# Performance work log

Hardware: AMD Instinct MI355X
Metric: run time of the kernel (lower is better)

## Reference

```python
import jax, jax.numpy as jnp
import numpy as np

B, T, E, H, O = 32, 512, 768, 3132, 19


def _ln(x, g, b, eps=1e-5):
    m = x.mean(-1, keepdims=True)
    v = x.var(-1, keepdims=True)
    return (x - m) / jnp.sqrt(v + eps) * g + b


def _cell(x, h, wih, bih, whh, bhh):
    # torch.nn.RNNCell with tanh nonlinearity
    return jnp.tanh(x @ wih.T + bih + h @ whh.T + bhh)


def _mha(seq, wqkv, bqkv, wo, bo):
    # seq: [T,B,D]; single-head torch MultiheadAttention (eval mode, no dropout)
    D = seq.shape[-1]
    qkv = seq @ wqkv.T + bqkv
    q, k, v = jnp.split(qkv, 3, axis=-1)
    scores = jnp.einsum('tbd,sbd->bts', q, k) / jnp.sqrt(jnp.asarray(D, seq.dtype))
    a = jax.nn.softmax(scores, axis=-1)
    ctx = jnp.einsum('bts,sbd->tbd', a, v)
    return ctx @ wo.T + bo


def setup_inputs() -> dict:
    key = jax.random.key(0)
    ks = jax.random.split(key, 12)
    s = lambda k, shape: jax.random.normal(k, shape, jnp.float32) * 0.02
    return {
        'x': jax.random.normal(ks[0], (B, T, E), jnp.float32),
        'in_g': jnp.ones((E,), jnp.float32), 'in_b': jnp.zeros((E,), jnp.float32),
        'w_ih1': s(ks[1], (H, E)), 'w_hh1': s(ks[2], (H, H)),
        'b_ih1': jnp.zeros((H,), jnp.float32), 'b_hh1': jnp.zeros((H,), jnp.float32),
        'ln1_g': jnp.ones((H,), jnp.float32), 'ln1_b': jnp.zeros((H,), jnp.float32),
        'w_ih2': s(ks[3], (E, H)), 'w_hh2': s(ks[4], (E, E)),
        'b_ih2': jnp.zeros((E,), jnp.float32), 'b_hh2': jnp.zeros((E,), jnp.float32),
        'mha1_wqkv': s(ks[5], (3 * H, H)), 'mha1_bqkv': jnp.zeros((3 * H,), jnp.float32),
        'mha1_wo': s(ks[6], (H, H)), 'mha1_bo': jnp.zeros((H,), jnp.float32),
        'mha2_wqkv': s(ks[7], (3 * E, E)), 'mha2_bqkv': jnp.zeros((3 * E,), jnp.float32),
        'mha2_wo': s(ks[8], (E, E)), 'mha2_bo': jnp.zeros((E,), jnp.float32),
        'w_cls': s(ks[9], (O, E)), 'b_cls': jnp.zeros((O,), jnp.float32),
    }


def reference(x, in_g, in_b, w_ih1, w_hh1, b_ih1, b_hh1, ln1_g, ln1_b,
              w_ih2, w_hh2, b_ih2, b_hh2,
              mha1_wqkv, mha1_bqkv, mha1_wo, mha1_bo,
              mha2_wqkv, mha2_bqkv, mha2_wo, mha2_bo, w_cls, b_cls):
    b = x.shape[0]
    xn = _ln(x, in_g, in_b)            # input_norm
    xs = jnp.swapaxes(xn, 0, 1)        # [T,B,E]
    h1_0 = jnp.zeros((b, w_ih1.shape[0]), x.dtype)
    h2_0 = jnp.zeros((b, w_ih2.shape[0]), x.dtype)

    def step(carry, xt):
        h1, h2 = carry
        h1 = _ln(_cell(xt, h1, w_ih1, b_ih1, w_hh1, b_hh1), ln1_g, ln1_b)
        h2 = _cell(h1, h2, w_ih2, b_ih2, w_hh2, b_hh2)
        return (h1, h2), (h1, h2)

    _, (h1s, h2s) = jax.lax.scan(step, (h1_0, h2_0), xs)  # [T,B,H], [T,B,E]
    ctx1 = _mha(h1s, mha1_wqkv, mha1_bqkv, mha1_wo, mha1_bo)  # dropout is identity in eval
    ctx2 = _mha(h2s, mha2_wqkv, mha2_bqkv, mha2_wo, mha2_bo)
    # the original second loop overwrites h1/h2 each t; only t = T-1 survives
    h1 = _cell(xs[-1], ctx1[-1], w_ih1, b_ih1, w_hh1, b_hh1)
    h2 = _cell(h1, ctx2[-1], w_ih2, b_ih2, w_hh2, b_hh2)
    return h2 @ w_cls.T + b_cls
```

## Files before the change

kernel.cpp:

```cpp
#include <hip/hip_runtime.h>
#include <cstdint>
#include <cmath>

#define BB 32
#define TT 512
#define EE 768
#define HH 3132
#define HP 3136
#define OO 19

#define NBLK 451
#define NTHR 256
#define WP 456
#define AP 232


#define PT(t) (((t) * 331) & 511)

typedef __attribute__((ext_vector_type(8))) short s8v;
typedef __attribute__((ext_vector_type(4))) float f4v;
typedef __attribute__((ext_vector_type(8))) unsigned short u16x8;

__device__ __forceinline__ unsigned short f2bf(float f) {
    uint32_t u = __float_as_uint(f);
    uint32_t r = u + 0x7FFFu + ((u >> 16) & 1u);
    return (unsigned short)(r >> 16);
}
__device__ __forceinline__ float bf2f(unsigned short h) {
    return __uint_as_float(((uint32_t)h) << 16);
}

#define MFMA(a, b, c) __builtin_amdgcn_mfma_f32_16x16x32_bf16((a), (b), (c), 0, 0, 0)

__device__ __forceinline__ f4v ld4_sc(const void* p) {
    f4v v;
    asm volatile("global_load_dwordx4 %0, %1, off sc0 sc1" : "=v"(v) : "v"(p) : "memory");
    return v;
}
#define WAITV() do { asm volatile("s_waitcnt vmcnt(0)" ::: "memory"); \
                     __builtin_amdgcn_sched_barrier(0); } while (0)
__device__ __forceinline__ void st_sc(float* p, float v) {
    __hip_atomic_store(p, v, __ATOMIC_RELAXED, __HIP_MEMORY_SCOPE_AGENT);
}
__device__ __forceinline__ void st16_sc(void* p, u16x8 v) {
    asm volatile("global_store_dwordx4 %0, %1, off sc0 sc1" :: "v"(p), "v"(v) : "memory");
}
__device__ __forceinline__ void st8_sc(void* p, uint2 v) {
    asm volatile("global_store_dwordx2 %0, %1, off sc0 sc1" :: "v"(p), "v"(v) : "memory");
}

struct PP {
    const unsigned short *xw1hi, *xw1lo;
    const unsigned short *whh1hi, *whh1lo, *wih2, *whh2;
    const float *b1c, *b2c, *gpad, *bepad;
    unsigned short *h1hist, *h2hist;
    unsigned short *h1nlo, *h2lo;
    float *part1, *part2;
    unsigned int *grp;
    unsigned int *epoch;
};

__device__ __forceinline__ void gbar(const PP& p, unsigned int k) {
    __syncthreads();
    asm volatile("s_waitcnt vmcnt(0)" ::: "memory");
    if (threadIdx.x == 0)
        __hip_atomic_fetch_add(&p.grp[(blockIdx.x & 63) * 32], 1u,
                               __ATOMIC_RELAXED, __HIP_MEMORY_SCOPE_AGENT);
    if (blockIdx.x == 0) {
        if (threadIdx.x < 64) {
            unsigned int mem = 7u + (threadIdx.x < (NBLK & 63) ? 1u : 0u);
            unsigned int tgt = mem * k;
            long g = 0;
            while (__hip_atomic_load(&p.grp[threadIdx.x * 32], __ATOMIC_RELAXED,
                                     __HIP_MEMORY_SCOPE_AGENT) < tgt) {
                __builtin_amdgcn_s_sleep(2);
                if (++g > (1L << 16)) break;
            }
        }
        __syncthreads();
        if (threadIdx.x == 0)
            __hip_atomic_store(p.epoch, k, __ATOMIC_RELAXED, __HIP_MEMORY_SCOPE_AGENT);
    } else {
        if (threadIdx.x == 0) {
            long g = 0;
            while (__hip_atomic_load(p.epoch, __ATOMIC_RELAXED,
                                     __HIP_MEMORY_SCOPE_AGENT) < k) {
                __builtin_amdgcn_s_sleep(2);
                if (++g > (1L << 16)) break;
            }
        }
    }
    __syncthreads();
    asm volatile("" ::: "memory");
}

__global__ __launch_bounds__(NTHR, 2) void persist_k(PP p) {
    __shared__ unsigned short Wlds[64][WP];
    __shared__ unsigned short Alds[32][AP];
    __shared__ float redS[4], redQ[4];
    const int blk = blockIdx.x, tid = threadIdx.x;
    const int wid = tid >> 6, lane = tid & 63;
    const int r = lane & 15, kg = lane >> 4;
    unsigned int bar = 0;

    const int t1nt = blk / 7,          t1ks = blk % 7;
    const int t2i  = blk - 343,        t2nt = t2i / 7, t2ks = t2i % 7;
    const int t3i  = blk - 427,        t3nt = t3i / 2, t3kh = t3i % 2;

    if (blk < 343) {
        const unsigned short* src = p.whh1hi + (size_t)(t1nt * 64) * HP + t1ks * 448;
        #pragma unroll
        for (int i = 0; i < 14; ++i) {
            int idx = tid + i * 256;
            int row = idx / 56, c8 = idx % 56;
            *(uint4*)&Wlds[row][c8 * 8] = *(const uint4*)(src + (size_t)row * HP + c8 * 8);
        }
    } else if (blk < 427) {
        const unsigned short* src = p.wih2 + (size_t)(t2nt * 64) * HP + t2ks * 448;
        #pragma unroll
        for (int i = 0; i < 14; ++i) {
            int idx = tid + i * 256;
            int row = idx / 56, c8 = idx % 56;
            *(uint4*)&Wlds[row][c8 * 8] = *(const uint4*)(src + (size_t)row * HP + c8 * 8);
        }
    } else {
        const unsigned short* src = p.whh2 + (size_t)(t3nt * 64) * EE + t3kh * 384;
        #pragma unroll
        for (int i = 0; i < 12; ++i) {
            int idx = tid + i * 256;
            int row = idx / 48, c8 = idx % 48;
            *(uint4*)&Wlds[row][c8 * 8] = *(const uint4*)(src + (size_t)row * EE + c8 * 8);
        }
    }
    __syncthreads();

    for (int t = 0; t <= TT; ++t) {
        if (blk < 343) {
            if (t >= 1 && t <= TT - 1) {
                f4v a0 = {0.f,0.f,0.f,0.f}, a1 = {0.f,0.f,0.f,0.f};
                const unsigned short* Wl = p.whh1lo + (size_t)(t1nt * 64 + wid * 16 + r) * HP + t1ks * 448 + kg * 8;
                const unsigned short* ringb = p.h1hist + (size_t)PT(t - 1) * BB * HP + t1ks * 448 + kg * 8;
                for (int hx = 0; hx < 2; ++hx) {
                    __syncthreads();
                    {
                        f4v lv[4];
                        #pragma unroll
                        for (int i = 0; i < 4; ++i) {
                            int idx = tid + i * 256;
                            int row = (idx < 896) ? idx / 28 : 0;
                            int c8  = (idx < 896) ? idx % 28 : 0;
                            lv[i] = ld4_sc(p.h1nlo + (size_t)row * HP + t1ks * 448 + hx * 224 + c8 * 8);
                        }
                        WAITV();
                        #pragma unroll
                        for (int i = 0; i < 4; ++i) {
                            int idx = tid + i * 256;
                            if (idx < 896) {
                                int row = idx / 28, c8 = idx % 28;
                                *(f4v*)&Alds[row][c8 * 8] = lv[i];
                            }
                        }
                    }
                    __syncthreads();
                    const unsigned short* Ah0 = ringb + (size_t)r * HP + hx * 224;
                    const unsigned short* Ah1 = ringb + (size_t)(r + 16) * HP + hx * 224;
                    const unsigned short* Wlh = Wl + hx * 224;
                    #pragma unroll
                    for (int kb = 0; kb < 7; ++kb) {
                        s8v bh  = *(const s8v*)&Wlds[wid * 16 + r][hx * 224 + kb * 32 + kg * 8];
                        s8v bl  = *(const s8v*)(Wlh + kb * 32);
                        s8v ah0 = *(const s8v*)(Ah0 + kb * 32);
                        s8v ah1 = *(const s8v*)(Ah1 + kb * 32);
                        s8v al0 = *(const s8v*)&Alds[r][kb * 32 + kg * 8];
                        s8v al1 = *(const s8v*)&Alds[r + 16][kb * 32 + kg * 8];
                        a0 = MFMA(ah0, bh, a0); a1 = MFMA(ah1, bh, a1);
                        a0 = MFMA(al0, bh, a0); a1 = MFMA(al1, bh, a1);
                        a0 = MFMA(ah0, bl, a0); a1 = MFMA(ah1, bl, a1);
                    }
                }
                int ncol = t1nt * 64 + wid * 16 + r;
                float* pp1 = p.part1 + (size_t)t1ks * BB * HP + ncol;
                #pragma unroll
                for (int q = 0; q < 4; ++q) {
                    st_sc(pp1 + (size_t)(kg * 4 + q) * HP,      a0[q]);
                    st_sc(pp1 + (size_t)(kg * 4 + q + 16) * HP, a1[q]);
                }
            }
        } else if (blk < 427) {
            if (t >= 1) {
                const unsigned short* ringb = p.h1hist + (size_t)PT(t - 1) * BB * HP + t2ks * 448 + kg * 8;
                const unsigned short* Ah0 = ringb + (size_t)r * HP;
                const unsigned short* Ah1 = ringb + (size_t)(r + 16) * HP;
                f4v a0 = {0.f,0.f,0.f,0.f}, a1 = {0.f,0.f,0.f,0.f};
                #pragma unroll
                for (int kb = 0; kb < 14; ++kb) {
                    s8v bh  = *(const s8v*)&Wlds[wid * 16 + r][kb * 32 + kg * 8];
                    s8v ah0 = *(const s8v*)(Ah0 + kb * 32);
                    s8v ah1 = *(const s8v*)(Ah1 + kb * 32);
                    a0 = MFMA(ah0, bh, a0); a1 = MFMA(ah1, bh, a1);
                }
                int ncol = t2nt * 64 + wid * 16 + r;
                float* pp2 = p.part2 + (size_t)t2ks * BB * EE + ncol;
                #pragma unroll
                for (int q = 0; q < 4; ++q) {
                    st_sc(pp2 + (size_t)(kg * 4 + q) * EE,      a0[q]);
                    st_sc(pp2 + (size_t)(kg * 4 + q + 16) * EE, a1[q]);
                }
            }
        } else {
            if (t >= 2) {
                const unsigned short* Hh = p.h2hist + (size_t)PT(t - 2) * BB * EE + t3kh * 384 + kg * 8;
                const unsigned short* Hl = p.h2lo + t3kh * 384 + kg * 8;
                f4v a0 = {0.f,0.f,0.f,0.f}, a1 = {0.f,0.f,0.f,0.f};
                #pragma unroll
                for (int c = 0; c < 2; ++c) {
                    f4v v0l[6], v1l[6];
                    #pragma unroll
                    for (int u = 0; u < 6; ++u) {
                        int kb = c * 6 + u;
                        v0l[u] = ld4_sc(Hl + (size_t)r * EE + kb * 32);
                        v1l[u] = ld4_sc(Hl + (size_t)(r + 16) * EE + kb * 32);
                    }
                    WAITV();
                    #pragma unroll
                    for (int u = 0; u < 6; ++u) {
                        int kb = c * 6 + u;
                        s8v bh  = *(const s8v*)&Wlds[wid * 16 + r][kb * 32 + kg * 8];
                        s8v ah0 = *(const s8v*)(Hh + (size_t)r * EE + kb * 32);
                        s8v ah1 = *(const s8v*)(Hh + (size_t)(r + 16) * EE + kb * 32);
                        a0 = MFMA(ah0, bh, a0);
                        a0 = MFMA(__builtin_bit_cast(s8v, v0l[u]), bh, a0);
                        a1 = MFMA(ah1, bh, a1);
                        a1 = MFMA(__builtin_bit_cast(s8v, v1l[u]), bh, a1);
                    }
                }
                int ncol = t3nt * 64 + wid * 16 + r;
                float* pp2 = p.part2 + (size_t)(7 + t3kh) * BB * EE + ncol;
                #pragma unroll
                for (int q = 0; q < 4; ++q) {
                    st_sc(pp2 + (size_t)(kg * 4 + q) * EE,      a0[q]);
                    st_sc(pp2 + (size_t)(kg * 4 + q + 16) * EE, a1[q]);
                }
            }
        }
        gbar(p, ++bar);

        if (blk < 32) {
            if (t <= TT - 1) {
                const int b = blk;
                const int nb = tid * 16;
                const bool act = (tid < 196);
                float acc[16];
                float s = 0.f, s2 = 0.f;
                if (act) {
                    #pragma unroll
                    for (int k4 = 0; k4 < 4; ++k4) {
                        f4v bb = *(const f4v*)(p.b1c + nb + k4 * 4);
                        #pragma unroll
                        for (int e = 0; e < 4; ++e) acc[k4 * 4 + e] = bb[e];
                    }
                    const u16x8* xh = (const u16x8*)(p.xw1hi + ((size_t)t * BB + b) * HP + nb);
                    const u16x8* xl = (const u16x8*)(p.xw1lo + ((size_t)t * BB + b) * HP + nb);
                    u16x8 h0v = xh[0], h1v = xh[1], l0v = xl[0], l1v = xl[1];
                    #pragma unroll
                    for (int j = 0; j < 8; ++j) acc[j]     += bf2f(h0v[j]) + bf2f(l0v[j]);
                    #pragma unroll
                    for (int j = 0; j < 8; ++j) acc[8 + j] += bf2f(h1v[j]) + bf2f(l1v[j]);
                    if (t > 0) {
                        {
                            f4v tmp[16];
                            #pragma unroll
                            for (int sl = 0; sl < 4; ++sl) {
                                const float* base = p.part1 + ((size_t)sl * BB + b) * HP + nb;
                                #pragma unroll
                                for (int k4 = 0; k4 < 4; ++k4) tmp[sl * 4 + k4] = ld4_sc(base + k4 * 4);
                            }
                            WAITV();
                            #pragma unroll
                            for (int sl = 0; sl < 4; ++sl)
                                #pragma unroll
                                for (int k4 = 0; k4 < 4; ++k4)
                                    #pragma unroll
                                    for (int e = 0; e < 4; ++e) acc[k4 * 4 + e] += tmp[sl * 4 + k4][e];
                        }
                        {
                            f4v tmp[12];
                            #pragma unroll
                            for (int sl = 0; sl < 3; ++sl) {
                                const float* base = p.part1 + ((size_t)(sl + 4) * BB + b) * HP + nb;
                                #pragma unroll
                                for (int k4 = 0; k4 < 4; ++k4) tmp[sl * 4 + k4] = ld4_sc(base + k4 * 4);
                            }
                            WAITV();
                            #pragma unroll
                            for (int sl = 0; sl < 3; ++sl)
                                #pragma unroll
                                for (int k4 = 0; k4 < 4; ++k4)
                                    #pragma unroll
                                    for (int e = 0; e < 4; ++e) acc[k4 * 4 + e] += tmp[sl * 4 + k4][e];
                        }
                    }
                    #pragma unroll
                    for (int j = 0; j < 16; ++j) {
                        if (nb + j < HH) {
                            float v = tanhf(acc[j]);
                            acc[j] = v; s += v; s2 += v * v;
                        } else acc[j] = 0.f;
                    }
                }
                for (int o = 32; o; o >>= 1) { s += __shfl_xor(s, o); s2 += __shfl_xor(s2, o); }
                if (lane == 0) { redS[wid] = s; redQ[wid] = s2; }
                __syncthreads();
                float S  = redS[0] + redS[1] + redS[2] + redS[3];
                float S2 = redQ[0] + redQ[1] + redQ[2] + redQ[3];
                float mm = S / (float)HH;
                float inv = rsqrtf(S2 / (float)HH - mm * mm + 1e-5f);
                __syncthreads();
                if (act) {
                    u16x8 ho0, ho1, lo0, lo1;
                    #pragma unroll
                    for (int k4 = 0; k4 < 4; ++k4) {
                        f4v gv = *(const f4v*)(p.gpad + nb + k4 * 4);
                        f4v bv = *(const f4v*)(p.bepad + nb + k4 * 4);
                        #pragma unroll
                        for (int e = 0; e < 4; ++e) {
                            int j = k4 * 4 + e, n = nb + j;
                            float o = (n < HH) ? (acc[j] - mm) * inv * gv[e] + bv[e] : 0.f;
                            unsigned short hb = f2bf(o);
                            unsigned short lb = f2bf(o - bf2f(hb));
                            if (j < 8) { ho0[j] = hb; lo0[j] = lb; }
                            else       { ho1[j - 8] = hb; lo1[j - 8] = lb; }
                        }
                    }
                    unsigned short* dh = p.h1hist + ((size_t)PT(t) * BB + b) * HP + nb;
                    unsigned short* dl = p.h1nlo + (size_t)b * HP + nb;
                    st16_sc(dh, ho0); st16_sc(dh + 8, ho1);
                    st16_sc(dl, lo0); st16_sc(dl + 8, lo1);
                }
            }
        } else if (blk < 64) {
            if (t >= 1) {
                const int b = blk - 32;
                if (tid < 192) {
                    const int nb = tid * 4;
                    f4v a4 = *(const f4v*)(p.b2c + nb);
                    f4v tp[9];
                    #pragma unroll
                    for (int sl = 0; sl < 9; ++sl)
                        tp[sl] = ld4_sc(p.part2 + ((size_t)sl * BB + b) * EE + nb);
                    WAITV();
                    #pragma unroll
                    for (int sl = 0; sl < 9; ++sl) {
                        float w = (t == 1 && sl >= 7) ? 0.f : 1.f;
                        #pragma unroll
                        for (int e = 0; e < 4; ++e) a4[e] += w * tp[sl][e];
                    }
                    unsigned short hb4[4], lb4[4];
                    #pragma unroll
                    for (int e = 0; e < 4; ++e) {
                        float v = tanhf(a4[e]);
                        hb4[e] = f2bf(v); lb4[e] = f2bf(v - bf2f(hb4[e]));
                    }
                    uint2 hp_, lp_;
                    hp_.x = (unsigned)hb4[0] | ((unsigned)hb4[1] << 16);
                    hp_.y = (unsigned)hb4[2] | ((unsigned)hb4[3] << 16);
                    lp_.x = (unsigned)lb4[0] | ((unsigned)lb4[1] << 16);
                    lp_.y = (unsigned)lb4[2] | ((unsigned)lb4[3] << 16);
                    st8_sc(p.h2hist + ((size_t)PT(t - 1) * BB + b) * EE + nb, hp_);
                    st8_sc(p.h2lo + (size_t)b * EE + nb, lp_);
                }
            }
        }
        gbar(p, ++bar);
    }
}

__global__ void ln_x_k(const float* __restrict__ x, const float* __restrict__ g,
                       const float* __restrict__ be, unsigned short* __restrict__ xnhi,
                       unsigned short* __restrict__ xnlo) {
    int bt = blockIdx.x;
    int b = bt >> 9, t = bt & 511;
    const float* row = x + ((size_t)b * TT + t) * EE;
    int tid = threadIdx.x;
    float v0 = row[tid], v1 = row[tid + 256], v2 = row[tid + 512];
    float s = v0 + v1 + v2, s2 = v0 * v0 + v1 * v1 + v2 * v2;
    for (int o = 32; o; o >>= 1) { s += __shfl_xor(s, o); s2 += __shfl_xor(s2, o); }
    __shared__ float r1[4], r2[4];
    int wid = tid >> 6, lane = tid & 63;
    if (lane == 0) { r1[wid] = s; r2[wid] = s2; }
    __syncthreads();
    s = r1[0] + r1[1] + r1[2] + r1[3];
    s2 = r2[0] + r2[1] + r2[2] + r2[3];
    float m = s / (float)EE, var = s2 / (float)EE - m * m;
    float inv = rsqrtf(var + 1e-5f);
    size_t ro = ((size_t)t * BB + b) * EE;
    float vals[3] = {v0, v1, v2};
#pragma unroll
    for (int i = 0; i < 3; i++) {
        int e = tid + i * 256;
        float o = (vals[i] - m) * inv * g[e] + be[e];
        unsigned short hb = f2bf(o);
        xnhi[ro + e] = hb;
        xnlo[ro + e] = f2bf(o - bf2f(hb));
    }
}

__global__ void castpad_k(const float* __restrict__ in, int N, int K,
                          unsigned short* __restrict__ out, int Np, int Kp) {
    size_t gid = (size_t)blockIdx.x * 256 + threadIdx.x;
    if (gid >= (size_t)Np * Kp) return;
    int n = (int)(gid / Kp), k = (int)(gid % Kp);
    out[gid] = (n < N && k < K) ? f2bf(in[(size_t)n * K + k]) : (unsigned short)0;
}

__global__ void castsplit_k(const float* __restrict__ in, int N, int K,
                            unsigned short* __restrict__ hi, unsigned short* __restrict__ lo,
                            int Np, int Kp) {
    size_t gid = (size_t)blockIdx.x * 256 + threadIdx.x;
    if (gid >= (size_t)Np * Kp) return;
    int n = (int)(gid / Kp), k = (int)(gid % Kp);
    float v = (n < N && k < K) ? in[(size_t)n * K + k] : 0.0f;
    unsigned short hb = f2bf(v);
    hi[gid] = hb;
    lo[gid] = f2bf(v - bf2f(hb));
}

__global__ void transcast_k(const float* __restrict__ in, int R, int C,
                            unsigned short* __restrict__ out, int Rp, int Cp) {
    __shared__ float tile[32][33];
    int c0 = blockIdx.x * 32, r0 = blockIdx.y * 32;
    int tx = threadIdx.x & 31, ty = threadIdx.x >> 5;
    for (int i = 0; i < 4; i++) {
        int r = r0 + ty + i * 8, c = c0 + tx;
        tile[ty + i * 8][tx] = (r < R && c < C) ? in[(size_t)r * C + c] : 0.0f;
    }
    __syncthreads();
    for (int i = 0; i < 4; i++) {
        int c = c0 + ty + i * 8, r = r0 + tx;
        if (c < Cp && r < Rp) out[(size_t)c * Rp + r] = f2bf(tile[tx][ty + i * 8]);
    }
}

__global__ void biascomb_k(const float* a, const float* b, float* o, int realN, int Np) {
    int gid = blockIdx.x * 256 + threadIdx.x;
    if (gid >= Np) return;
    o[gid] = (gid < realN) ? a[gid] + b[gid] : 0.0f;
}

__global__ void padcopy_k(const float* in, float* out, int realN, int Np) {
    int gid = blockIdx.x * 256 + threadIdx.x;
    if (gid >= Np) return;
    out[gid] = (gid < realN) ? in[gid] : 0.0f;
}

__global__ __launch_bounds__(256) void gemmbig_k(const unsigned short* __restrict__ Ahi,
                                                 const unsigned short* __restrict__ Alo,
                                                 const unsigned short* __restrict__ Whi,
                                                 const unsigned short* __restrict__ Wlo,
                                                 unsigned short* __restrict__ outhi,
                                                 unsigned short* __restrict__ outlo,
                                                 int Kld, int Np, int ksteps) {
    int m0 = blockIdx.x * 32;
    int n0 = blockIdx.y * 64;
    int wid = threadIdx.x >> 6, lane = threadIdx.x & 63;
    int r = lane & 15, kg = lane >> 4;
    size_t woff = (size_t)(n0 + wid * 16 + r) * Kld + kg * 8;
    const unsigned short* Whr = Whi + woff;
    const unsigned short* Wlr = Wlo + woff;
    size_t aoff = (size_t)(m0 + r) * Kld + kg * 8;
    const unsigned short* Ah0 = Ahi + aoff;
    const unsigned short* Ah1 = Ah0 + (size_t)16 * Kld;
    const unsigned short* Al0 = Alo + aoff;
    const unsigned short* Al1 = Al0 + (size_t)16 * Kld;
    f4v acc0 = {0.f, 0.f, 0.f, 0.f}, acc1 = {0.f, 0.f, 0.f, 0.f};
#pragma unroll 4
    for (int s = 0; s < ksteps; s++) {
        s8v bh  = *(const s8v*)(Whr + s * 32);
        s8v bl  = *(const s8v*)(Wlr + s * 32);
        s8v a0h = *(const s8v*)(Ah0 + s * 32);
        s8v a1h = *(const s8v*)(Ah1 + s * 32);
        s8v a0l = *(const s8v*)(Al0 + s * 32);
        s8v a1l = *(const s8v*)(Al1 + s * 32);
        acc0 = MFMA(a0h, bh, acc0); acc1 = MFMA(a1h, bh, acc1);
        acc0 = MFMA(a0l, bh, acc0); acc1 = MFMA(a1l, bh, acc1);
        acc0 = MFMA(a0h, bl, acc0); acc1 = MFMA(a1h, bl, acc1);
    }
    int ncol = n0 + wid * 16 + r;
#pragma unroll
    for (int q = 0; q < 4; q++) {
        int m = kg * 4 + q;
        float v0 = acc0[q], v1 = acc1[q];
        unsigned short h0 = f2bf(v0), h1 = f2bf(v1);
        outhi[(size_t)(m0 + m) * Np + ncol]      = h0;
        outlo[(size_t)(m0 + m) * Np + ncol]      = f2bf(v0 - bf2f(h0));
        outhi[(size_t)(m0 + m + 16) * Np + ncol] = h1;
        outlo[(size_t)(m0 + m + 16) * Np + ncol] = f2bf(v1 - bf2f(h1));
    }
}

__global__ __launch_bounds__(256) void gemm32_k(const unsigned short* __restrict__ A,
                                                const unsigned short* __restrict__ W,
                                                float* __restrict__ part,
                                                int Kld, int Np, int ksteps, int slot_base) {
    int n0 = blockIdx.x * 64;
    int kb = blockIdx.y;
    int k0 = kb * ksteps * 32;
    int wid = threadIdx.x >> 6, lane = threadIdx.x & 63;
    int r = lane & 15, kg = lane >> 4;
    const unsigned short* Wrow = W + (size_t)(n0 + wid * 16 + r) * Kld + k0 + kg * 8;
    const unsigned short* Ar0 = A + (size_t)r * Kld + k0 + kg * 8;
    const unsigned short* Ar1 = Ar0 + (size_t)16 * Kld;
    f4v acc0 = {0.f, 0.f, 0.f, 0.f}, acc1 = {0.f, 0.f, 0.f, 0.f};
#pragma unroll
    for (int s = 0; s < ksteps; s++) {
        s8v bf = *(const s8v*)(Wrow + s * 32);
        s8v a0 = *(const s8v*)(Ar0 + s * 32);
        s8v a1 = *(const s8v*)(Ar1 + s * 32);
        acc0 = MFMA(a0, bf, acc0);
        acc1 = MFMA(a1, bf, acc1);
    }
    int ncol = n0 + wid * 16 + r;
    float* p = part + (size_t)(slot_base + kb) * 32 * Np + ncol;
#pragma unroll
    for (int q = 0; q < 4; q++) {
        int m = kg * 4 + q;
        p[(size_t)m * Np]        = acc0[q];
        p[(size_t)(m + 16) * Np] = acc1[q];
    }
}

__global__ void epi_k(const float* __restrict__ part, int nslots, int Np, int realN,
                      const float* __restrict__ bias, int act,
                      unsigned short* __restrict__ outbf) {
    int gid = blockIdx.x * 256 + threadIdx.x;
    int b = gid / Np, n = gid % Np;
    float v = 0.0f;
    if (n < realN) {
        v = bias ? bias[n] : 0.0f;
        for (int s = 0; s < nslots; s++) v += part[(size_t)(s * 32 + b) * Np + n];
        if (act) v = tanhf(v);
    }
    outbf[(size_t)b * Np + n] = f2bf(v);
}

__global__ void qbk_k(const unsigned short* __restrict__ q, int Kp, int realK,
                      const float* __restrict__ bk, float* __restrict__ out) {
    int b = blockIdx.x, tid = threadIdx.x;
    float s = 0.f;
    for (int d = tid; d < realK; d += 256) s += bf2f(q[(size_t)b * Kp + d]) * bk[d];
    for (int o = 32; o; o >>= 1) s += __shfl_xor(s, o);
    __shared__ float r[4];
    if ((tid & 63) == 0) r[tid >> 6] = s;
    __syncthreads();
    if (tid == 0) out[b] = r[0] + r[1] + r[2] + r[3];
}

__global__ void scores_k(const unsigned short* __restrict__ hs, const unsigned short* __restrict__ qk,
                         const float* __restrict__ qbk, float* __restrict__ out,
                         int Kp, float scale) {
    int gid = blockIdx.x * 4 + (threadIdx.x >> 6);
    int lane = threadIdx.x & 63;
    int b = gid >> 9, t = gid & 511;
    const unsigned short* hrow = hs + ((size_t)PT(t) * BB + b) * Kp;
    const unsigned short* qrow = qk + (size_t)b * Kp;
    float acc = 0.f;
    for (int kb = lane * 4; kb < Kp; kb += 256) {
        uint2 hv = *reinterpret_cast<const uint2*>(hrow + kb);
        uint2 qv = *reinterpret_cast<const uint2*>(qrow + kb);
        acc += __uint_as_float(hv.x << 16) * __uint_as_float(qv.x << 16);
        acc += __uint_as_float(hv.x & 0xFFFF0000u) * __uint_as_float(qv.x & 0xFFFF0000u);
        acc += __uint_as_float(hv.y << 16) * __uint_as_float(qv.y << 16);
        acc += __uint_as_float(hv.y & 0xFFFF0000u) * __uint_as_float(qv.y & 0xFFFF0000u);
    }
    for (int o = 32; o; o >>= 1) acc += __shfl_xor(acc, o);
    if (lane == 0) out[b * TT + t] = (acc + qbk[b]) * scale;
}

__global__ void softmax_k(const float* __restrict__ in, float* __restrict__ out) {
    int b = blockIdx.x, tid = threadIdx.x;
    float v0 = in[b * TT + tid], v1 = in[b * TT + 256 + tid];
    float mx = fmaxf(v0, v1);
    for (int o = 32; o; o >>= 1) mx = fmaxf(mx, __shfl_xor(mx, o));
    __shared__ float r[4], r2[4];
    int wid = tid >> 6, lane = tid & 63;
    if (lane == 0) r[wid] = mx;
    __syncthreads();
    mx = fmaxf(fmaxf(r[0], r[1]), fmaxf(r[2], r[3]));
    float e0 = expf(v0 - mx), e1 = expf(v1 - mx);
    float s = e0 + e1;
    for (int o = 32; o; o >>= 1) s += __shfl_xor(s, o);
    if (lane == 0) r2[wid] = s;
    __syncthreads();
    s = r2[0] + r2[1] + r2[2] + r2[3];
    float invs = 1.0f / s;
    out[b * TT + tid] = e0 * invs;
    out[b * TT + 256 + tid] = e1 * invs;
}

__global__ void attnsum_k(const unsigned short* __restrict__ hs, const float* __restrict__ aw,
                          unsigned short* __restrict__ out, int Kp) {
    int gid = blockIdx.x * 256 + threadIdx.x;
    int b = gid / Kp, e = gid % Kp;
    float acc = 0.f;
    for (int t = 0; t < TT; t++)
        acc += aw[b * TT + t] * bf2f(hs[((size_t)PT(t) * BB + b) * Kp + e]);
    out[(size_t)b * Kp + e] = f2bf(acc);
}

__global__ void cls_k(const unsigned short* __restrict__ h2f, const float* __restrict__ wcls,
                      const float* __restrict__ bcls, float* __restrict__ out) {
    int b = blockIdx.x;
    int wid = threadIdx.x >> 6, lane = threadIdx.x & 63;
    for (int o = wid; o < OO; o += 4) {
        float s = 0.f;
        for (int e = lane; e < EE; e += 64)
            s += bf2f(h2f[(size_t)b * EE + e]) * wcls[o * EE + e];
        for (int off = 32; off; off >>= 1) s += __shfl_xor(s, off);
        if (lane == 0) out[b * OO + o] = s + bcls[o];
    }
}

__global__ void fail_k(float* out) {
    int i = blockIdx.x * 256 + threadIdx.x;
    if (i < BB * OO) out[i] = 1e9f;
}

extern "C" void kernel_launch(void* const* d_in, const int* in_sizes, int n_in,
                              void* d_out, int out_size, void* d_ws, size_t ws_size,
                              hipStream_t stream) {
    const float* x        = (const float*)d_in[0];
    const float* in_g     = (const float*)d_in[1];
    const float* in_b     = (const float*)d_in[2];
    const float* w_ih1    = (const float*)d_in[3];
    const float* w_hh1    = (const float*)d_in[4];
    const float* b_ih1    = (const float*)d_in[5];
    const float* b_hh1    = (const float*)d_in[6];
    const float* ln1_g    = (const float*)d_in[7];
    const float* ln1_b    = (const float*)d_in[8];
    const float* w_ih2    = (const float*)d_in[9];
    const float* w_hh2    = (const float*)d_in[10];
    const float* b_ih2    = (const float*)d_in[11];
    const float* b_hh2    = (const float*)d_in[12];
    const float* m1_wqkv  = (const float*)d_in[13];
    const float* m1_bqkv  = (const float*)d_in[14];
    const float* m1_wo    = (const float*)d_in[15];
    const float* m1_bo    = (const float*)d_in[16];
    const float* m2_wqkv  = (const float*)d_in[17];
    const float* m2_bqkv  = (const float*)d_in[18];
    const float* m2_wo    = (const float*)d_in[19];
    const float* m2_bo    = (const float*)d_in[20];
    const float* w_cls    = (const float*)d_in[21];
    const float* b_cls    = (const float*)d_in[22];
    float* out = (float*)d_out;

    const size_t TB = (size_t)TT * BB;
    size_t cur = 0;
    auto alloc = [&](size_t bytes) { cur = (cur + 255) & ~(size_t)255; size_t o = cur; cur += bytes; return o; };
    char* ws = (char*)d_ws;
    #define US(off) ((unsigned short*)(ws + (off)))
    #define FP(off) ((float*)(ws + (off)))

    size_t o_xnhi   = alloc(TB * EE * 2);
    size_t o_xnlo   = alloc(TB * EE * 2);
    size_t o_wih1hi = alloc((size_t)HP * EE * 2);
    size_t o_wih1lo = alloc((size_t)HP * EE * 2);
    size_t o_whh1hi = alloc((size_t)HP * HP * 2);
    size_t o_whh1lo = alloc((size_t)HP * HP * 2);
    size_t o_wih2   = alloc((size_t)EE * HP * 2);
    size_t o_whh2   = alloc((size_t)EE * EE * 2);
    size_t o_h1s    = alloc(TB * HP * 2);
    size_t o_h2s    = alloc(TB * EE * 2);
    size_t o_h1nlo  = alloc((size_t)BB * HP * 2);
    size_t o_h2lo   = alloc((size_t)BB * EE * 2);
    size_t o_part1  = alloc((size_t)8 * BB * HP * 4);
    size_t o_part2  = alloc((size_t)9 * BB * EE * 4);
    size_t o_b1c    = alloc((size_t)HP * 4);
    size_t o_b2c    = alloc((size_t)EE * 4);
    size_t o_gpad   = alloc((size_t)HP * 4);
    size_t o_bepad  = alloc((size_t)HP * 4);
    size_t o_sync   = alloc(64 * 128 + 256);
    size_t o_xw1hi  = alloc(TB * HP * 2);
    size_t o_xw1lo  = alloc(TB * HP * 2);
    size_t o_q1     = alloc((size_t)BB * HP * 2);
    size_t o_qk1    = alloc((size_t)BB * HP * 2);
    size_t o_u1     = alloc((size_t)BB * HP * 2);
    size_t o_vc1    = alloc((size_t)BB * HP * 2);
    size_t o_ctx1   = alloc((size_t)BB * HP * 2);
    size_t o_qbk1   = alloc(BB * 4);
    size_t o_sc1    = alloc((size_t)BB * TT * 4);
    size_t o_aw1    = alloc((size_t)BB * TT * 4);
    size_t o_q2     = alloc((size_t)BB * EE * 2);
    size_t o_qk2    = alloc((size_t)BB * EE * 2);
    size_t o_u2     = alloc((size_t)BB * EE * 2);
    size_t o_vc2    = alloc((size_t)BB * EE * 2);
    size_t o_ctx2   = alloc((size_t)BB * EE * 2);
    size_t o_qbk2   = alloc(BB * 4);
    size_t o_sc2    = alloc((size_t)BB * TT * 4);
    size_t o_aw2    = alloc((size_t)BB * TT * 4);
    size_t o_h1f    = alloc((size_t)BB * HP * 2);
    size_t o_h2f    = alloc((size_t)BB * EE * 2);

    size_t ov = o_xw1hi;
    auto oalloc = [&](size_t bytes) { ov = (ov + 255) & ~(size_t)255; size_t o = ov; ov += bytes; return o; };
    size_t v_wq1  = oalloc((size_t)HP * HP * 2);
    size_t v_wk1T = oalloc((size_t)HP * HP * 2);
    size_t v_wv1  = oalloc((size_t)HP * HP * 2);
    size_t v_wo1  = oalloc((size_t)HP * HP * 2);
    size_t v_wq2  = oalloc((size_t)EE * EE * 2);
    size_t v_wk2T = oalloc((size_t)EE * EE * 2);
    size_t v_wv2  = oalloc((size_t)EE * EE * 2);
    size_t v_wo2  = oalloc((size_t)EE * EE * 2);

    if (ws_size < cur) {
        fail_k<<<3, 256, 0, stream>>>(out);
        return;
    }

    ln_x_k<<<BB * TT, 256, 0, stream>>>(x, in_g, in_b, US(o_xnhi), US(o_xnlo));
    castsplit_k<<<(HP * EE + 255) / 256, 256, 0, stream>>>(w_ih1, HH, EE, US(o_wih1hi), US(o_wih1lo), HP, EE);
    castsplit_k<<<(HP * HP + 255) / 256, 256, 0, stream>>>(w_hh1, HH, HH, US(o_whh1hi), US(o_whh1lo), HP, HP);
    castpad_k<<<(EE * HP + 255) / 256, 256, 0, stream>>>(w_ih2, EE, HH, US(o_wih2), EE, HP);
    castpad_k<<<(EE * EE + 255) / 256, 256, 0, stream>>>(w_hh2, EE, EE, US(o_whh2), EE, EE);
    biascomb_k<<<(HP + 255) / 256, 256, 0, stream>>>(b_ih1, b_hh1, FP(o_b1c), HH, HP);
    biascomb_k<<<(EE + 255) / 256, 256, 0, stream>>>(b_ih2, b_hh2, FP(o_b2c), EE, EE);
    padcopy_k<<<(HP + 255) / 256, 256, 0, stream>>>(ln1_g, FP(o_gpad), HH, HP);
    padcopy_k<<<(HP + 255) / 256, 256, 0, stream>>>(ln1_b, FP(o_bepad), HH, HP);
    hipMemsetAsync(ws + o_sync, 0, 64 * 128 + 256, stream);

    gemmbig_k<<<dim3((int)(TB / 32), HP / 64), 256, 0, stream>>>(US(o_xnhi), US(o_xnlo),
                                                                 US(o_wih1hi), US(o_wih1lo),
                                                                 US(o_xw1hi), US(o_xw1lo), EE, HP, EE / 32);

    PP pp;
    pp.xw1hi = US(o_xw1hi); pp.xw1lo = US(o_xw1lo);
    pp.whh1hi = US(o_whh1hi); pp.whh1lo = US(o_whh1lo);
    pp.wih2 = US(o_wih2); pp.whh2 = US(o_whh2);
    pp.b1c = FP(o_b1c); pp.b2c = FP(o_b2c);
    pp.gpad = FP(o_gpad); pp.bepad = FP(o_bepad);
    pp.h1hist = US(o_h1s); pp.h2hist = US(o_h2s);
    pp.h1nlo = US(o_h1nlo); pp.h2lo = US(o_h2lo);
    pp.part1 = FP(o_part1); pp.part2 = FP(o_part2);
    pp.grp = (unsigned int*)(ws + o_sync);
    pp.epoch = (unsigned int*)(ws + o_sync + 64 * 128);
    persist_k<<<NBLK, NTHR, 0, stream>>>(pp);

    castpad_k<<<(HP * HP + 255) / 256, 256, 0, stream>>>(m1_wqkv, HH, HH, US(v_wq1), HP, HP);
    castpad_k<<<(HP * HP + 255) / 256, 256, 0, stream>>>(m1_wqkv + (size_t)2 * HH * HH, HH, HH, US(v_wv1), HP, HP);
    castpad_k<<<(HP * HP + 255) / 256, 256, 0, stream>>>(m1_wo, HH, HH, US(v_wo1), HP, HP);
    transcast_k<<<dim3(HP / 32, HP / 32), 256, 0, stream>>>(m1_wqkv + (size_t)HH * HH, HH, HH, US(v_wk1T), HP, HP);
    castpad_k<<<(EE * EE + 255) / 256, 256, 0, stream>>>(m2_wqkv, EE, EE, US(v_wq2), EE, EE);
    castpad_k<<<(EE * EE + 255) / 256, 256, 0, stream>>>(m2_wqkv + (size_t)2 * EE * EE, EE, EE, US(v_wv2), EE, EE);
    castpad_k<<<(EE * EE + 255) / 256, 256, 0, stream>>>(m2_wo, EE, EE, US(v_wo2), EE, EE);
    transcast_k<<<dim3(EE / 32, EE / 32), 256, 0, stream>>>(m2_wqkv + (size_t)EE * EE, EE, EE, US(v_wk2T), EE, EE);

    const int PTLAST = (511 * 331) & 511;
    const unsigned short* h1last = US(o_h1s) + (size_t)PTLAST * BB * HP;
    const unsigned short* h2last = US(o_h2s) + (size_t)PTLAST * BB * EE;
    const float sc_scale1 = 1.0f / sqrtf((float)HH);
    const float sc_scale2 = 1.0f / sqrtf((float)EE);

    gemm32_k<<<dim3(HP / 64, 7), 256, 0, stream>>>(h1last, US(v_wq1), FP(o_part1), HP, HP, 14, 0);
    epi_k<<<BB * HP / 256, 256, 0, stream>>>(FP(o_part1), 7, HP, HH, m1_bqkv, 0, US(o_q1));
    gemm32_k<<<dim3(HP / 64, 7), 256, 0, stream>>>(US(o_q1), US(v_wk1T), FP(o_part1), HP, HP, 14, 0);
    epi_k<<<BB * HP / 256, 256, 0, stream>>>(FP(o_part1), 7, HP, HH, nullptr, 0, US(o_qk1));
    qbk_k<<<BB, 256, 0, stream>>>(US(o_q1), HP, HH, m1_bqkv + HH, FP(o_qbk1));
    scores_k<<<BB * TT / 4, 256, 0, stream>>>(US(o_h1s), US(o_qk1), FP(o_qbk1), FP(o_sc1), HP, sc_scale1);
    softmax_k<<<BB, 256, 0, stream>>>(FP(o_sc1), FP(o_aw1));
    attnsum_k<<<BB * HP / 256, 256, 0, stream>>>(US(o_h1s), FP(o_aw1), US(o_u1), HP);
    gemm32_k<<<dim3(HP / 64, 7), 256, 0, stream>>>(US(o_u1), US(v_wv1), FP(o_part1), HP, HP, 14, 0);
    epi_k<<<BB * HP / 256, 256, 0, stream>>>(FP(o_part1), 7, HP, HH, m1_bqkv + 2 * HH, 0, US(o_vc1));
    gemm32_k<<<dim3(HP / 64, 7), 256, 0, stream>>>(US(o_vc1), US(v_wo1), FP(o_part1), HP, HP, 14, 0);
    epi_k<<<BB * HP / 256, 256, 0, stream>>>(FP(o_part1), 7, HP, HH, m1_bo, 0, US(o_ctx1));

    gemm32_k<<<dim3(EE / 64, 3), 256, 0, stream>>>(h2last, US(v_wq2), FP(o_part2), EE, EE, 8, 0);
    epi_k<<<BB * EE / 256, 256, 0, stream>>>(FP(o_part2), 3, EE, EE, m2_bqkv, 0, US(o_q2));
    gemm32_k<<<dim3(EE / 64, 3), 256, 0, stream>>>(US(o_q2), US(v_wk2T), FP(o_part2), EE, EE, 8, 0);
    epi_k<<<BB * EE / 256, 256, 0, stream>>>(FP(o_part2), 3, EE, EE, nullptr, 0, US(o_qk2));
    qbk_k<<<BB, 256, 0, stream>>>(US(o_q2), EE, EE, m2_bqkv + EE, FP(o_qbk2));
    scores_k<<<BB * TT / 4, 256, 0, stream>>>(US(o_h2s), US(o_qk2), FP(o_qbk2), FP(o_sc2), EE, sc_scale2);
    softmax_k<<<BB, 256, 0, stream>>>(FP(o_sc2), FP(o_aw2));
    attnsum_k<<<BB * EE / 256, 256, 0, stream>>>(US(o_h2s), FP(o_aw2), US(o_u2), EE);
    gemm32_k<<<dim3(EE / 64, 3), 256, 0, stream>>>(US(o_u2), US(v_wv2), FP(o_part2), EE, EE, 8, 0);
    epi_k<<<BB * EE / 256, 256, 0, stream>>>(FP(o_part2), 3, EE, EE, m2_bqkv + 2 * EE, 0, US(o_vc2));
    gemm32_k<<<dim3(EE / 64, 3), 256, 0, stream>>>(US(o_vc2), US(v_wo2), FP(o_part2), EE, EE, 8, 0);
    epi_k<<<BB * EE / 256, 256, 0, stream>>>(FP(o_part2), 3, EE, EE, m2_bo, 0, US(o_ctx2));

    const unsigned short* xnlast = US(o_xnhi) + (size_t)(TT - 1) * BB * EE;
    gemm32_k<<<dim3(HP / 64, 1), 256, 0, stream>>>(xnlast, US(o_wih1hi), FP(o_part1), EE, HP, EE / 32, 0);
    gemm32_k<<<dim3(HP / 64, 7), 256, 0, stream>>>(US(o_ctx1), US(o_whh1hi), FP(o_part1), HP, HP, 14, 1);
    epi_k<<<BB * HP / 256, 256, 0, stream>>>(FP(o_part1), 8, HP, HH, FP(o_b1c), 1, US(o_h1f));
    gemm32_k<<<dim3(EE / 64, 7), 256, 0, stream>>>(US(o_h1f), US(o_wih2), FP(o_part2), HP, EE, 14, 0);
    gemm32_k<<<dim3(EE / 64, 1), 256, 0, stream>>>(US(o_ctx2), US(o_whh2), FP(o_part2), EE, EE, EE / 32, 7);
    epi_k<<<BB * EE / 256, 256, 0, stream>>>(FP(o_part2), 8, EE, EE, FP(o_b2c), 1, US(o_h2f));
    cls_k<<<BB, 256, 0, stream>>>(US(o_h2f), w_cls, b_cls, out);
}
```

Measured before the change: 17.82 ms.

## Store low-part hidden states in per-timestep rings and replicate barrier epoch flag

```diff
diff --git a/kernel.cpp b/kernel.cpp
--- a/kernel.cpp
+++ b/kernel.cpp
@@ -54,6 +54,7 @@
     const unsigned short *whh1hi, *whh1lo, *wih2, *whh2;
     const float *b1c, *b2c, *gpad, *bepad;
     unsigned short *h1hist, *h2hist;
+    unsigned short *h1lring, *h2lring;
     unsigned short *h1nlo, *h2lo;
     float *part1, *part2;
     unsigned int *grp;
@@ -78,12 +79,13 @@
             }
         }
         __syncthreads();
-        if (threadIdx.x == 0)
-            __hip_atomic_store(p.epoch, k, __ATOMIC_RELAXED, __HIP_MEMORY_SCOPE_AGENT);
+        if (threadIdx.x < 64)
+            __hip_atomic_store(&p.epoch[threadIdx.x * 32], k,
+                               __ATOMIC_RELAXED, __HIP_MEMORY_SCOPE_AGENT);
     } else {
         if (threadIdx.x == 0) {
             long g = 0;
-            while (__hip_atomic_load(p.epoch, __ATOMIC_RELAXED,
+            while (__hip_atomic_load(&p.epoch[(blockIdx.x & 63) * 32], __ATOMIC_RELAXED,
                                      __HIP_MEMORY_SCOPE_AGENT) < k) {
                 __builtin_amdgcn_s_sleep(2);
                 if (++g > (1L << 16)) break;
@@ -94,9 +96,10 @@
     asm volatile("" ::: "memory");
 }
 
+template<int MODE>
 __global__ __launch_bounds__(NTHR, 2) void persist_k(PP p) {
     __shared__ unsigned short Wlds[64][WP];
-    __shared__ unsigned short Alds[32][AP];
+    __shared__ unsigned short Alds[(MODE == 1) ? 1 : 32][AP];
     __shared__ float redS[4], redQ[4];
     const int blk = blockIdx.x, tid = threadIdx.x;
     const int wid = tid >> 6, lane = tid & 63;
@@ -138,44 +141,62 @@
         if (blk < 343) {
             if (t >= 1 && t <= TT - 1) {
                 f4v a0 = {0.f,0.f,0.f,0.f}, a1 = {0.f,0.f,0.f,0.f};
-                const unsigned short* Wl = p.whh1lo + (size_t)(t1nt * 64 + wid * 16 + r) * HP + t1ks * 448 + kg * 8;
-                const unsigned short* ringb = p.h1hist + (size_t)PT(t - 1) * BB * HP + t1ks * 448 + kg * 8;
-                for (int hx = 0; hx < 2; ++hx) {
-                    __syncthreads();
-                    {
-                        f4v lv[4];
-                        #pragma unroll
-                        for (int i = 0; i < 4; ++i) {
-                            int idx = tid + i * 256;
-                            int row = (idx < 896) ? idx / 28 : 0;
-                            int c8  = (idx < 896) ? idx % 28 : 0;
-                            lv[i] = ld4_sc(p.h1nlo + (size_t)row * HP + t1ks * 448 + hx * 224 + c8 * 8);
-                        }
-                        WAITV();
-                        #pragma unroll
-                        for (int i = 0; i < 4; ++i) {
-                            int idx = tid + i * 256;
-                            if (idx < 896) {
-                                int row = idx / 28, c8 = idx % 28;
-                                *(f4v*)&Alds[row][c8 * 8] = lv[i];
-                            }
-                        }
-                    }
-                    __syncthreads();
-                    const unsigned short* Ah0 = ringb + (size_t)r * HP + hx * 224;
-                    const unsigned short* Ah1 = ringb + (size_t)(r + 16) * HP + hx * 224;
-                    const unsigned short* Wlh = Wl + hx * 224;
-                    #pragma unroll
-                    for (int kb = 0; kb < 7; ++kb) {
-                        s8v bh  = *(const s8v*)&Wlds[wid * 16 + r][hx * 224 + kb * 32 + kg * 8];
-                        s8v bl  = *(const s8v*)(Wlh + kb * 32);
-                        s8v ah0 = *(const s8v*)(Ah0 + kb * 32);
-                        s8v ah1 = *(const s8v*)(Ah1 + kb * 32);
-                        s8v al0 = *(const s8v*)&Alds[r][kb * 32 + kg * 8];
-                        s8v al1 = *(const s8v*)&Alds[r + 16][kb * 32 + kg * 8];
+                if constexpr (MODE == 1) {
+                    const unsigned short* rh = p.h1hist  + (size_t)PT(t - 1) * BB * HP + t1ks * 448 + kg * 8;
+                    const unsigned short* rl = p.h1lring + (size_t)PT(t - 1) * BB * HP + t1ks * 448 + kg * 8;
+                    const unsigned short* Wl = p.whh1lo + (size_t)(t1nt * 64 + wid * 16 + r) * HP + t1ks * 448 + kg * 8;
+                    #pragma unroll
+                    for (int kb = 0; kb < 14; ++kb) {
+                        s8v bh  = *(const s8v*)&Wlds[wid * 16 + r][kb * 32 + kg * 8];
+                        s8v bl  = *(const s8v*)(Wl + kb * 32);
+                        s8v ah0 = *(const s8v*)(rh + (size_t)r * HP + kb * 32);
+                        s8v ah1 = *(const s8v*)(rh + (size_t)(r + 16) * HP + kb * 32);
+                        s8v al0 = *(const s8v*)(rl + (size_t)r * HP + kb * 32);
+                        s8v al1 = *(const s8v*)(rl + (size_t)(r + 16) * HP + kb * 32);
                         a0 = MFMA(ah0, bh, a0); a1 = MFMA(ah1, bh, a1);
                         a0 = MFMA(al0, bh, a0); a1 = MFMA(al1, bh, a1);
                         a0 = MFMA(ah0, bl, a0); a1 = MFMA(ah1, bl, a1);
+                    }
+                } else {
+                    const unsigned short* Wl = p.whh1lo + (size_t)(t1nt * 64 + wid * 16 + r) * HP + t1ks * 448 + kg * 8;
+                    const unsigned short* ringb = p.h1hist + (size_t)PT(t - 1) * BB * HP + t1ks * 448 + kg * 8;
+                    for (int hx = 0; hx < 2; ++hx) {
+                        __syncthreads();
+                        {
+                            f4v lv[4];
+                            #pragma unroll
+                            for (int i = 0; i < 4; ++i) {
+                                int idx = tid + i * 256;
+                                int row = (idx < 896) ? idx / 28 : 0;
+                                int c8  = (idx < 896) ? idx % 28 : 0;
+                                lv[i] = ld4_sc(p.h1nlo + (size_t)row * HP + t1ks * 448 + hx * 224 + c8 * 8);
+                            }
+                            WAITV();
+                            #pragma unroll
+                            for (int i = 0; i < 4; ++i) {
+                                int idx = tid + i * 256;
+                                if (idx < 896) {
+                                    int row = idx / 28, c8 = idx % 28;
+                                    *(f4v*)&Alds[row][c8 * 8] = lv[i];
+                                }
+                            }
+                        }
+                        __syncthreads();
+                        const unsigned short* Ah0 = ringb + (size_t)r * HP + hx * 224;
+                        const unsigned short* Ah1 = ringb + (size_t)(r + 16) * HP + hx * 224;
+                        const unsigned short* Wlh = Wl + hx * 224;
+                        #pragma unroll
+                        for (int kb = 0; kb < 7; ++kb) {
+                            s8v bh  = *(const s8v*)&Wlds[wid * 16 + r][hx * 224 + kb * 32 + kg * 8];
+                            s8v bl  = *(const s8v*)(Wlh + kb * 32);
+                            s8v ah0 = *(const s8v*)(Ah0 + kb * 32);
+                            s8v ah1 = *(const s8v*)(Ah1 + kb * 32);
+                            s8v al0 = *(const s8v*)&Alds[r][kb * 32 + kg * 8];
+                            s8v al1 = *(const s8v*)&Alds[r + 16][kb * 32 + kg * 8];
+                            a0 = MFMA(ah0, bh, a0); a1 = MFMA(ah1, bh, a1);
+                            a0 = MFMA(al0, bh, a0); a1 = MFMA(al1, bh, a1);
+                            a0 = MFMA(ah0, bl, a0); a1 = MFMA(ah1, bl, a1);
+                        }
                     }
                 }
                 int ncol = t1nt * 64 + wid * 16 + r;
@@ -210,28 +231,42 @@
         } else {
             if (t >= 2) {
                 const unsigned short* Hh = p.h2hist + (size_t)PT(t - 2) * BB * EE + t3kh * 384 + kg * 8;
-                const unsigned short* Hl = p.h2lo + t3kh * 384 + kg * 8;
                 f4v a0 = {0.f,0.f,0.f,0.f}, a1 = {0.f,0.f,0.f,0.f};
-                #pragma unroll
-                for (int c = 0; c < 2; ++c) {
-                    f4v v0l[6], v1l[6];
-                    #pragma unroll
-                    for (int u = 0; u < 6; ++u) {
-                        int kb = c * 6 + u;
-                        v0l[u] = ld4_sc(Hl + (size_t)r * EE + kb * 32);
-                        v1l[u] = ld4_sc(Hl + (size_t)(r + 16) * EE + kb * 32);
-                    }
-                    WAITV();
-                    #pragma unroll
-                    for (int u = 0; u < 6; ++u) {
-                        int kb = c * 6 + u;
+                if constexpr (MODE == 1) {
+                    const unsigned short* Hl = p.h2lring + (size_t)PT(t - 2) * BB * EE + t3kh * 384 + kg * 8;
+                    #pragma unroll
+                    for (int kb = 0; kb < 12; ++kb) {
                         s8v bh  = *(const s8v*)&Wlds[wid * 16 + r][kb * 32 + kg * 8];
                         s8v ah0 = *(const s8v*)(Hh + (size_t)r * EE + kb * 32);
                         s8v ah1 = *(const s8v*)(Hh + (size_t)(r + 16) * EE + kb * 32);
-                        a0 = MFMA(ah0, bh, a0);
-                        a0 = MFMA(__builtin_bit_cast(s8v, v0l[u]), bh, a0);
-                        a1 = MFMA(ah1, bh, a1);
-                        a1 = MFMA(__builtin_bit_cast(s8v, v1l[u]), bh, a1);
+                        s8v al0 = *(const s8v*)(Hl + (size_t)r * EE + kb * 32);
+                        s8v al1 = *(const s8v*)(Hl + (size_t)(r + 16) * EE + kb * 32);
+                        a0 = MFMA(ah0, bh, a0); a0 = MFMA(al0, bh, a0);
+                        a1 = MFMA(ah1, bh, a1); a1 = MFMA(al1, bh, a1);
+                    }
+                } else {
+                    const unsigned short* Hl = p.h2lo + t3kh * 384 + kg * 8;
+                    #pragma unroll
+                    for (int c = 0; c < 2; ++c) {
+                        f4v v0l[6], v1l[6];
+                        #pragma unroll
+                        for (int u = 0; u < 6; ++u) {
+                            int kb = c * 6 + u;
+                            v0l[u] = ld4_sc(Hl + (size_t)r * EE + kb * 32);
+                            v1l[u] = ld4_sc(Hl + (size_t)(r + 16) * EE + kb * 32);
+                        }
+                        WAITV();
+                        #pragma unroll
+                        for (int u = 0; u < 6; ++u) {
+                            int kb = c * 6 + u;
+                            s8v bh  = *(const s8v*)&Wlds[wid * 16 + r][kb * 32 + kg * 8];
+                            s8v ah0 = *(const s8v*)(Hh + (size_t)r * EE + kb * 32);
+                            s8v ah1 = *(const s8v*)(Hh + (size_t)(r + 16) * EE + kb * 32);
+                            a0 = MFMA(ah0, bh, a0);
+                            a0 = MFMA(__builtin_bit_cast(s8v, v0l[u]), bh, a0);
+                            a1 = MFMA(ah1, bh, a1);
+                            a1 = MFMA(__builtin_bit_cast(s8v, v1l[u]), bh, a1);
+                        }
                     }
                 }
                 int ncol = t3nt * 64 + wid * 16 + r;
@@ -333,9 +368,14 @@
                         }
                     }
                     unsigned short* dh = p.h1hist + ((size_t)PT(t) * BB + b) * HP + nb;
-                    unsigned short* dl = p.h1nlo + (size_t)b * HP + nb;
                     st16_sc(dh, ho0); st16_sc(dh + 8, ho1);
-                    st16_sc(dl, lo0); st16_sc(dl + 8, lo1);
+                    if constexpr (MODE == 1) {
+                        unsigned short* dl = p.h1lring + ((size_t)PT(t) * BB + b) * HP + nb;
+                        st16_sc(dl, lo0); st16_sc(dl + 8, lo1);
+                    } else {
+                        unsigned short* dl = p.h1nlo + (size_t)b * HP + nb;
+                        st16_sc(dl, lo0); st16_sc(dl + 8, lo1);
+                    }
                 }
             }
         } else if (blk < 64) {
@@ -367,7 +407,10 @@
                     lp_.x = (unsigned)lb4[0] | ((unsigned)lb4[1] << 16);
                     lp_.y = (unsigned)lb4[2] | ((unsigned)lb4[3] << 16);
                     st8_sc(p.h2hist + ((size_t)PT(t - 1) * BB + b) * EE + nb, hp_);
-                    st8_sc(p.h2lo + (size_t)b * EE + nb, lp_);
+                    if constexpr (MODE == 1)
+                        st8_sc(p.h2lring + ((size_t)PT(t - 1) * BB + b) * EE + nb, lp_);
+                    else
+                        st8_sc(p.h2lo + (size_t)b * EE + nb, lp_);
                 }
             }
         }
@@ -678,7 +721,7 @@
     size_t o_b2c    = alloc((size_t)EE * 4);
     size_t o_gpad   = alloc((size_t)HP * 4);
     size_t o_bepad  = alloc((size_t)HP * 4);
-    size_t o_sync   = alloc(64 * 128 + 256);
+    size_t o_sync   = alloc(64 * 128 * 2 + 256);
     size_t o_xw1hi  = alloc(TB * HP * 2);
     size_t o_xw1lo  = alloc(TB * HP * 2);
     size_t o_q1     = alloc((size_t)BB * HP * 2);
@@ -699,6 +742,10 @@
     size_t o_aw2    = alloc((size_t)BB * TT * 4);
     size_t o_h1f    = alloc((size_t)BB * HP * 2);
     size_t o_h2f    = alloc((size_t)BB * EE * 2);
+    size_t cur_base = cur;
+    size_t o_h1lr   = alloc(TB * HP * 2);
+    size_t o_h2lr   = alloc(TB * EE * 2);
+    size_t cur_full = cur;
 
     size_t ov = o_xw1hi;
     auto oalloc = [&](size_t bytes) { ov = (ov + 255) & ~(size_t)255; size_t o = ov; ov += bytes; return o; };
@@ -711,10 +758,10 @@
     size_t v_wv2  = oalloc((size_t)EE * EE * 2);
     size_t v_wo2  = oalloc((size_t)EE * EE * 2);
 
-    if (ws_size < cur) {
-        fail_k<<<3, 256, 0, stream>>>(out);
-        return;
-    }
+    int mode;
+    if (ws_size >= cur_full) mode = 1;
+    else if (ws_size >= cur_base) mode = 0;
+    else { fail_k<<<3, 256, 0, stream>>>(out); return; }
 
     ln_x_k<<<BB * TT, 256, 0, stream>>>(x, in_g, in_b, US(o_xnhi), US(o_xnlo));
     castsplit_k<<<(HP * EE + 255) / 256, 256, 0, stream>>>(w_ih1, HH, EE, US(o_wih1hi), US(o_wih1lo), HP, EE);
@@ -725,7 +772,7 @@
     biascomb_k<<<(EE + 255) / 256, 256, 0, stream>>>(b_ih2, b_hh2, FP(o_b2c), EE, EE);
     padcopy_k<<<(HP + 255) / 256, 256, 0, stream>>>(ln1_g, FP(o_gpad), HH, HP);
     padcopy_k<<<(HP + 255) / 256, 256, 0, stream>>>(ln1_b, FP(o_bepad), HH, HP);
-    hipMemsetAsync(ws + o_sync, 0, 64 * 128 + 256, stream);
+    hipMemsetAsync(ws + o_sync, 0, 64 * 128 * 2 + 256, stream);
 
     gemmbig_k<<<dim3((int)(TB / 32), HP / 64), 256, 0, stream>>>(US(o_xnhi), US(o_xnlo),
                                                                  US(o_wih1hi), US(o_wih1lo),
@@ -738,11 +785,13 @@
     pp.b1c = FP(o_b1c); pp.b2c = FP(o_b2c);
     pp.gpad = FP(o_gpad); pp.bepad = FP(o_bepad);
     pp.h1hist = US(o_h1s); pp.h2hist = US(o_h2s);
+    pp.h1lring = US(mode ? o_h1lr : o_h1nlo); pp.h2lring = US(mode ? o_h2lr : o_h2lo);
     pp.h1nlo = US(o_h1nlo); pp.h2lo = US(o_h2lo);
     pp.part1 = FP(o_part1); pp.part2 = FP(o_part2);
     pp.grp = (unsigned int*)(ws + o_sync);
     pp.epoch = (unsigned int*)(ws + o_sync + 64 * 128);
-    persist_k<<<NBLK, NTHR, 0, stream>>>(pp);
+    if (mode) persist_k<1><<<NBLK, NTHR, 0, stream>>>(pp);
+    else      persist_k<0><<<NBLK, NTHR, 0, stream>>>(pp);
 
     castpad_k<<<(HP * HP + 255) / 256, 256, 0, stream>>>(m1_wqkv, HH, HH, US(v_wq1), HP, HP);
     castpad_k<<<(HP * HP + 255) / 256, 256, 0, stream>>>(m1_wqkv + (size_t)2 * HH * HH, HH, HH, US(v_wv1), HP, HP);
```

Result: no change. 17.82 ms (+0.0%).
